# Kernel tuning notes

Measured on AMD Instinct MI355X. Metric: run time of the kernel, lower is better.

Reference implementation:

```python
import jax, jax.numpy as jnp
import numpy as np

NUM_USERS = 50000
NUM_ITEMS = 50000
N = NUM_USERS + NUM_ITEMS
EMBED_K = 64
N_LAYERS = 3
FEAT = 2048
N_EDGES = 2000000
BATCH = 8192
LEAKY_SLOPE = 0.2


def _l2norm(x):
    # torch F.normalize(p=2, dim=1): x / max(||x||, 1e-12)
    return x / jnp.maximum(jnp.linalg.norm(x, axis=1, keepdims=True), 1e-12)


def setup_inputs():
    key = jax.random.key(0)
    ks = jax.random.split(key, 12)
    s = 1.0 / np.sqrt(EMBED_K)
    return {
        "Gu": jax.random.normal(ks[0], (NUM_USERS, EMBED_K), jnp.float32) * 0.1,
        "Gi": jax.random.normal(ks[1], (NUM_ITEMS, EMBED_K), jnp.float32) * 0.1,
        "Tu": jax.random.normal(ks[2], (NUM_USERS, EMBED_K), jnp.float32) * 0.1,
        "F": jax.random.uniform(ks[3], (NUM_ITEMS, FEAT), jnp.float32),
        "proj_w": jax.random.normal(ks[4], (EMBED_K, FEAT), jnp.float32) / np.sqrt(FEAT),
        "proj_b": jnp.zeros((EMBED_K,), jnp.float32),
        "W1": jax.random.normal(ks[5], (N_LAYERS, EMBED_K, EMBED_K), jnp.float32) * s,
        "b1": jnp.zeros((N_LAYERS, EMBED_K), jnp.float32),
        "W2": jax.random.normal(ks[6], (N_LAYERS, EMBED_K, EMBED_K), jnp.float32) * s,
        "b2": jnp.zeros((N_LAYERS, EMBED_K), jnp.float32),
        "edge_weight": jax.random.uniform(ks[7], (N_EDGES,), jnp.float32) * 0.05,
        "edge_index": jax.random.randint(ks[8], (2, N_EDGES), 0, N, jnp.int32),
        "users": jax.random.randint(ks[9], (BATCH,), 0, NUM_USERS, jnp.int32),
        "items": jax.random.randint(ks[10], (BATCH,), 0, NUM_ITEMS, jnp.int32),
    }


def _propagate(Gu, Gi, W1, b1, W2, b2, edge_weight, edge_index):
    src, dst = edge_index[0], edge_index[1]
    x = jnp.concatenate([Gu, Gi], axis=0)  # [N, d]
    embs = [x]
    for l in range(N_LAYERS):
        # sparse adjacency aggregation: agg = A_hat @ x
        msg = x[src] * edge_weight[:, None]              # [E, d]
        agg = jax.ops.segment_sum(msg, dst, num_segments=N)  # [N, d]
        # NGCF layer: W1(x + agg) + W2(x * agg), leaky relu
        h = (x + agg) @ W1[l].T + b1[l] + (x * agg) @ W2[l].T + b2[l]
        h = jax.nn.leaky_relu(h, LEAKY_SLOPE)
        # dropout p=0 (identity), then per-node L2 normalize
        h = _l2norm(h)
        embs.append(h)
        x = h
    all_e = jnp.mean(jnp.stack(embs, axis=1), axis=1)  # mean over layers
    return all_e[:NUM_USERS], all_e[NUM_USERS:]


def reference(Gu, Gi, Tu, F, proj_w, proj_b, W1, b1, W2, b2, edge_weight, edge_index, users, items):
    gu, gi = _propagate(Gu, Gi, W1, b1, W2, b2, edge_weight, edge_index)
    gamma_u = gu[users]          # [B, d]
    gamma_i = gi[items]          # [B, d]
    theta_u = Tu[users]          # [B, d]
    proj_i = _l2norm(F[items] @ proj_w.T + proj_b)  # [B, d]
    xui = jnp.sum(gamma_u * gamma_i, axis=1) + jnp.sum(theta_u * proj_i, axis=1)
    return xui
```

## Files before the change

### kernel.cpp

```cpp
#include <hip/hip_runtime.h>

#define NUSERS 50000
#define NITEMS 50000
#define NN (NUSERS + NITEMS)
#define KDIM 64
#define NLAYERS 3
#define FEAT 2048
#define NEDGES 2000000
#define BATCH 8192
#define SLOPE 0.2f

#define BSLOT 64
#define CNT_PAD 100352
#define XBLK 6250
#define CBLK 98
#define TBLK 512
#define NNK (NN * KDIM)

typedef __attribute__((ext_vector_type(8))) short bf16x8;
typedef __attribute__((ext_vector_type(4))) float f32x4;

union U8 {
    bf16x8 v;
    uint4 u;
};

__device__ __forceinline__ unsigned short f2bf(float f) {
    unsigned int u = __float_as_uint(f);
    unsigned int r = (u + 0x7fffu + ((u >> 16) & 1u)) >> 16;
    return (unsigned short)r;
}
__device__ __forceinline__ unsigned int pack2(float a, float b) {
    return (unsigned int)f2bf(a) | ((unsigned int)f2bf(b) << 16);
}
__device__ __forceinline__ float b2f(unsigned short h) {
    return __uint_as_float((unsigned int)h << 16);
}

__global__ __launch_bounds__(256) void setup_kernel(const float* __restrict__ Gu,
                                                    const float* __restrict__ Gi,
                                                    const float* __restrict__ pw,
                                                    unsigned short* __restrict__ xh,
                                                    int* __restrict__ cnt,
                                                    unsigned short* __restrict__ pwh) {
    int bx = blockIdx.x;
    if (bx < XBLK) {
        int i = bx * 256 + threadIdx.x;
        const int totalU = NUSERS * KDIM / 4;
        float4 v = (i < totalU) ? ((const float4*)Gu)[i] : ((const float4*)Gi)[i - totalU];
        ushort4 h;
        h.x = f2bf(v.x); h.y = f2bf(v.y); h.z = f2bf(v.z); h.w = f2bf(v.w);
        ((ushort4*)xh)[i] = h;
    } else if (bx < XBLK + CBLK) {
        int i = (bx - XBLK) * 256 + threadIdx.x;
        ((int4*)cnt)[i] = make_int4(0, 0, 0, 0);
    } else {
        int tid = (bx - XBLK - CBLK) * 256 + threadIdx.x;
        pwh[tid] = f2bf(pw[tid]);
    }
}

__global__ __launch_bounds__(256) void fill_fixed_kernel(const int* __restrict__ ei,
                                                         const float* __restrict__ ew,
                                                         int* __restrict__ cnt,
                                                         int2* __restrict__ bucket) {
    int e = blockIdx.x * blockDim.x + threadIdx.x;
    if (e >= NEDGES) return;
    int src = ei[e];
    int dst = ei[NEDGES + e];
    int slot = atomicAdd(&cnt[dst], 1);
    if (slot < BSLOT)
        bucket[((long long)dst << 6) + slot] = make_int2(src, __float_as_int(ew[e]));
}

__global__ __launch_bounds__(256) void agg_kernel(const unsigned short* __restrict__ xh,
                                                  const int2* __restrict__ bucket,
                                                  const int* __restrict__ cnt,
                                                  unsigned short* __restrict__ aggh) {
    int t = threadIdx.x;
    int lane = t & 63, wid = t >> 6;
    int g = lane >> 3, l8 = lane & 7;
    int n = (blockIdx.x * 4 + wid) * 8 + g;
    if (n >= NN) return;
    int m = cnt[n];
    if (m > BSLOT) m = BSLOT;
    const int2* bk = bucket + ((long long)n << 6);
    const uint4* x4 = (const uint4*)xh;
    float a0[8], a1[8], a2[8], a3[8];
#pragma unroll
    for (int q = 0; q < 8; ++q) { a0[q] = 0.f; a1[q] = 0.f; a2[q] = 0.f; a3[q] = 0.f; }
    int j = 0;
    for (; j + 4 <= m; j += 4) {
        int2 p0 = bk[j], p1 = bk[j + 1], p2 = bk[j + 2], p3 = bk[j + 3];
        uint4 u0 = x4[((long long)p0.x << 3) + l8];
        uint4 u1 = x4[((long long)p1.x << 3) + l8];
        uint4 u2 = x4[((long long)p2.x << 3) + l8];
        uint4 u3 = x4[((long long)p3.x << 3) + l8];
        float w0 = __int_as_float(p0.y), w1 = __int_as_float(p1.y);
        float w2 = __int_as_float(p2.y), w3 = __int_as_float(p3.y);
        a0[0] += w0 * __uint_as_float(u0.x << 16); a0[1] += w0 * __uint_as_float(u0.x & 0xFFFF0000u);
        a0[2] += w0 * __uint_as_float(u0.y << 16); a0[3] += w0 * __uint_as_float(u0.y & 0xFFFF0000u);
        a0[4] += w0 * __uint_as_float(u0.z << 16); a0[5] += w0 * __uint_as_float(u0.z & 0xFFFF0000u);
        a0[6] += w0 * __uint_as_float(u0.w << 16); a0[7] += w0 * __uint_as_float(u0.w & 0xFFFF0000u);
        a1[0] += w1 * __uint_as_float(u1.x << 16); a1[1] += w1 * __uint_as_float(u1.x & 0xFFFF0000u);
        a1[2] += w1 * __uint_as_float(u1.y << 16); a1[3] += w1 * __uint_as_float(u1.y & 0xFFFF0000u);
        a1[4] += w1 * __uint_as_float(u1.z << 16); a1[5] += w1 * __uint_as_float(u1.z & 0xFFFF0000u);
        a1[6] += w1 * __uint_as_float(u1.w << 16); a1[7] += w1 * __uint_as_float(u1.w & 0xFFFF0000u);
        a2[0] += w2 * __uint_as_float(u2.x << 16); a2[1] += w2 * __uint_as_float(u2.x & 0xFFFF0000u);
        a2[2] += w2 * __uint_as_float(u2.y << 16); a2[3] += w2 * __uint_as_float(u2.y & 0xFFFF0000u);
        a2[4] += w2 * __uint_as_float(u2.z << 16); a2[5] += w2 * __uint_as_float(u2.z & 0xFFFF0000u);
        a2[6] += w2 * __uint_as_float(u2.w << 16); a2[7] += w2 * __uint_as_float(u2.w & 0xFFFF0000u);
        a3[0] += w3 * __uint_as_float(u3.x << 16); a3[1] += w3 * __uint_as_float(u3.x & 0xFFFF0000u);
        a3[2] += w3 * __uint_as_float(u3.y << 16); a3[3] += w3 * __uint_as_float(u3.y & 0xFFFF0000u);
        a3[4] += w3 * __uint_as_float(u3.z << 16); a3[5] += w3 * __uint_as_float(u3.z & 0xFFFF0000u);
        a3[6] += w3 * __uint_as_float(u3.w << 16); a3[7] += w3 * __uint_as_float(u3.w & 0xFFFF0000u);
    }
    for (; j < m; ++j) {
        int2 p0 = bk[j];
        uint4 u0 = x4[((long long)p0.x << 3) + l8];
        float w0 = __int_as_float(p0.y);
        a0[0] += w0 * __uint_as_float(u0.x << 16); a0[1] += w0 * __uint_as_float(u0.x & 0xFFFF0000u);
        a0[2] += w0 * __uint_as_float(u0.y << 16); a0[3] += w0 * __uint_as_float(u0.y & 0xFFFF0000u);
        a0[4] += w0 * __uint_as_float(u0.z << 16); a0[5] += w0 * __uint_as_float(u0.z & 0xFFFF0000u);
        a0[6] += w0 * __uint_as_float(u0.w << 16); a0[7] += w0 * __uint_as_float(u0.w & 0xFFFF0000u);
    }
#pragma unroll
    for (int q = 0; q < 8; ++q) a0[q] = (a0[q] + a1[q]) + (a2[q] + a3[q]);
    uint4 o;
    o.x = pack2(a0[0], a0[1]); o.y = pack2(a0[2], a0[3]);
    o.z = pack2(a0[4], a0[5]); o.w = pack2(a0[6], a0[7]);
    *(uint4*)(aggh + (long long)n * KDIM + l8 * 8) = o;
}

__global__ __launch_bounds__(256) void gemm_layer_kernel(const unsigned short* __restrict__ xh_in,
                                                         const unsigned short* __restrict__ aggh,
                                                         const float* __restrict__ W1,
                                                         const float* __restrict__ b1,
                                                         const float* __restrict__ W2,
                                                         const float* __restrict__ b2,
                                                         unsigned short* __restrict__ xhout,
                                                         int layer) {
    __shared__ unsigned short sS[64 * 72];
    __shared__ unsigned short sP[64 * 72];
    __shared__ unsigned short sW1[64 * 72];
    __shared__ unsigned short sW2[64 * 72];
    int t = threadIdx.x;
    const float* W1g = W1 + (long long)layer * KDIM * KDIM;
    const float* W2g = W2 + (long long)layer * KDIM * KDIM;
    for (int idx = t; idx < KDIM * KDIM; idx += 256) {
        int j = idx >> 6, k = idx & 63;
        sW1[j * 72 + k] = f2bf(W1g[idx]);
        sW2[j * 72 + k] = f2bf(W2g[idx]);
    }
    int n0 = blockIdx.x * 64;
    {
        int r = t >> 2, q = t & 3;
        int node = n0 + r;
        unsigned short* dS = &sS[r * 72 + q * 16];
        unsigned short* dP = &sP[r * 72 + q * 16];
        if (node < NN) {
            const unsigned short* xb = xh_in + (long long)node * KDIM + q * 16;
            const unsigned short* ab = aggh + (long long)node * KDIM + q * 16;
            uint4 hx = *(const uint4*)xb;
            uint4 hx2 = *(const uint4*)(xb + 8);
            uint4 ha = *(const uint4*)ab;
            uint4 ha2 = *(const uint4*)(ab + 8);
            uint4 swv, pwv, swv2, pwv2;
#define PROC(XW, AW, SW, PW)                                                        \
            {                                                                       \
                float xx0 = __uint_as_float((XW) << 16);                            \
                float xx1 = __uint_as_float((XW) & 0xFFFF0000u);                    \
                float aa0 = __uint_as_float((AW) << 16);                            \
                float aa1 = __uint_as_float((AW) & 0xFFFF0000u);                    \
                SW = pack2(xx0 + aa0, xx1 + aa1);                                   \
                PW = pack2(xx0 * aa0, xx1 * aa1);                                   \
            }
            PROC(hx.x, ha.x, swv.x, pwv.x)
            PROC(hx.y, ha.y, swv.y, pwv.y)
            PROC(hx.z, ha.z, swv.z, pwv.z)
            PROC(hx.w, ha.w, swv.w, pwv.w)
            PROC(hx2.x, ha2.x, swv2.x, pwv2.x)
            PROC(hx2.y, ha2.y, swv2.y, pwv2.y)
            PROC(hx2.z, ha2.z, swv2.z, pwv2.z)
            PROC(hx2.w, ha2.w, swv2.w, pwv2.w)
#undef PROC
            *(uint4*)dS = swv;
            *(uint4*)(dS + 8) = swv2;
            *(uint4*)dP = pwv;
            *(uint4*)(dP + 8) = pwv2;
        } else {
            uint4 z = make_uint4(0, 0, 0, 0);
            *(uint4*)dS = z; *(uint4*)(dS + 8) = z;
            *(uint4*)dP = z; *(uint4*)(dP + 8) = z;
        }
    }
    __syncthreads();

    int l = t & 63, w = t >> 6, m16 = l & 15, g4 = l >> 4;
    f32x4 acc[4];
#pragma unroll
    for (int c = 0; c < 4; ++c) {
        float bb = b1[layer * KDIM + c * 16 + m16] + b2[layer * KDIM + c * 16 + m16];
        acc[c] = (f32x4){bb, bb, bb, bb};
    }
    const int abase = (w * 16 + m16) * 72;
#pragma unroll
    for (int kh = 0; kh < 2; ++kh) {
        int ko = kh * 32 + g4 * 8;
        bf16x8 aS = *(const bf16x8*)&sS[abase + ko];
        bf16x8 aP = *(const bf16x8*)&sP[abase + ko];
#pragma unroll
        for (int c = 0; c < 4; ++c) {
            bf16x8 bw1 = *(const bf16x8*)&sW1[(c * 16 + m16) * 72 + ko];
            acc[c] = __builtin_amdgcn_mfma_f32_16x16x32_bf16(aS, bw1, acc[c], 0, 0, 0);
            bf16x8 bw2 = *(const bf16x8*)&sW2[(c * 16 + m16) * 72 + ko];
            acc[c] = __builtin_amdgcn_mfma_f32_16x16x32_bf16(aP, bw2, acc[c], 0, 0, 0);
        }
    }

    float sq[4] = {0.f, 0.f, 0.f, 0.f};
#pragma unroll
    for (int c = 0; c < 4; ++c) {
#pragma unroll
        for (int reg = 0; reg < 4; ++reg) {
            float h = acc[c][reg];
            h = h > 0.f ? h : SLOPE * h;
            acc[c][reg] = h;
            sq[reg] += h * h;
        }
    }
#pragma unroll
    for (int reg = 0; reg < 4; ++reg) {
#pragma unroll
        for (int off = 1; off < 16; off <<= 1) sq[reg] += __shfl_xor(sq[reg], off);
        sq[reg] = 1.0f / fmaxf(sqrtf(sq[reg]), 1e-12f);
    }
#pragma unroll
    for (int reg = 0; reg < 4; ++reg) {
        int node = n0 + w * 16 + g4 * 4 + reg;
        if (node < NN) {
#pragma unroll
            for (int c = 0; c < 4; ++c)
                xhout[(long long)node * KDIM + c * 16 + m16] = f2bf(acc[c][reg] * sq[reg]);
        }
    }
}

__global__ __launch_bounds__(512) void proj_kernel(const float* __restrict__ F,
                                                   const unsigned short* __restrict__ pwh,
                                                   const float* __restrict__ pb,
                                                   const int* __restrict__ items,
                                                   float* __restrict__ projB) {
    __shared__ float lds[8][64][16];
    int t = threadIdx.x;
    int l = t & 63, w = t >> 6, m16 = l & 15, g4 = l >> 4;
    int i0 = blockIdx.x * 16;
    int item = items[i0 + m16];
    const float* frow = F + (long long)item * FEAT + g4 * 8;
    f32x4 acc[4];
#pragma unroll
    for (int c = 0; c < 4; ++c) acc[c] = (f32x4){0.f, 0.f, 0.f, 0.f};
    float4 fa[8], fb[8];
#pragma unroll
    for (int u = 0; u < 8; ++u) {
        const float* p = frow + (w * 8 + u) * 32;
        fa[u] = *(const float4*)p;
        fb[u] = *(const float4*)(p + 4);
    }
#pragma unroll
    for (int u = 0; u < 8; ++u) {
        U8 af;
        af.u = make_uint4(pack2(fa[u].x, fa[u].y), pack2(fa[u].z, fa[u].w),
                          pack2(fb[u].x, fb[u].y), pack2(fb[u].z, fb[u].w));
#pragma unroll
        for (int c = 0; c < 4; ++c) {
            bf16x8 bw = *(const bf16x8*)(pwh + (long long)(c * 16 + m16) * FEAT +
                                         (w * 8 + u) * 32 + g4 * 8);
            acc[c] = __builtin_amdgcn_mfma_f32_16x16x32_bf16(af.v, bw, acc[c], 0, 0, 0);
        }
    }
#pragma unroll
    for (int c = 0; c < 4; ++c)
#pragma unroll
        for (int reg = 0; reg < 4; ++reg) lds[w][l][c * 4 + reg] = acc[c][reg];
    __syncthreads();
    for (int e = t; e < 1024; e += 512) {
        int ll = e >> 4, v = e & 15;
        float s = lds[0][ll][v];
#pragma unroll
        for (int ww = 1; ww < 8; ++ww) s += lds[ww][ll][v];
        lds[0][ll][v] = s;
    }
    __syncthreads();
    if (w == 0) {
        float av[4][4];
        float sq[4] = {0.f, 0.f, 0.f, 0.f};
#pragma unroll
        for (int c = 0; c < 4; ++c) {
            float bb = pb[c * 16 + m16];
#pragma unroll
            for (int reg = 0; reg < 4; ++reg) {
                float h = lds[0][l][c * 4 + reg] + bb;
                av[c][reg] = h;
                sq[reg] += h * h;
            }
        }
#pragma unroll
        for (int reg = 0; reg < 4; ++reg) {
#pragma unroll
            for (int off = 1; off < 16; off <<= 1) sq[reg] += __shfl_xor(sq[reg], off);
            sq[reg] = 1.0f / fmaxf(sqrtf(sq[reg]), 1e-12f);
        }
#pragma unroll
        for (int reg = 0; reg < 4; ++reg) {
            int b = i0 + g4 * 4 + reg;
#pragma unroll
            for (int c = 0; c < 4; ++c)
                projB[(long long)b * KDIM + c * 16 + m16] = av[c][reg] * sq[reg];
        }
    }
}

__global__ __launch_bounds__(256) void final_kernel(const unsigned short* __restrict__ xh0,
                                                    const unsigned short* __restrict__ xh1,
                                                    const unsigned short* __restrict__ xh2,
                                                    const unsigned short* __restrict__ xh3,
                                                    const float* __restrict__ Tu,
                                                    const float* __restrict__ projB,
                                                    const int* __restrict__ users,
                                                    const int* __restrict__ items,
                                                    float* __restrict__ out) {
    int lane = threadIdx.x & 63;
    int wid = threadIdx.x >> 6;
    int b = blockIdx.x * 4 + wid;
    if (b >= BATCH) return;
    int u = users[b];
    int it = NUSERS + items[b];
    long long uo = (long long)u * KDIM + lane;
    long long io = (long long)it * KDIM + lane;
    float gu = b2f(xh0[uo]) + b2f(xh1[uo]) + b2f(xh2[uo]) + b2f(xh3[uo]);
    float gi = b2f(xh0[io]) + b2f(xh1[io]) + b2f(xh2[io]) + b2f(xh3[io]);
    float tu = Tu[(long long)u * KDIM + lane];
    float pi = projB[(long long)b * KDIM + lane];
    float v = gu * gi * (1.0f / 16.0f) + tu * pi;
#pragma unroll
    for (int off = 32; off > 0; off >>= 1) v += __shfl_xor(v, off);
    if (lane == 0) out[b] = v;
}

extern "C" void kernel_launch(void* const* d_in, const int* in_sizes, int n_in,
                              void* d_out, int out_size, void* d_ws, size_t ws_size,
                              hipStream_t stream) {
    const float* Gu = (const float*)d_in[0];
    const float* Gi = (const float*)d_in[1];
    const float* Tu = (const float*)d_in[2];
    const float* F = (const float*)d_in[3];
    const float* pw = (const float*)d_in[4];
    const float* pb = (const float*)d_in[5];
    const float* W1 = (const float*)d_in[6];
    const float* b1 = (const float*)d_in[7];
    const float* W2 = (const float*)d_in[8];
    const float* b2 = (const float*)d_in[9];
    const float* ew = (const float*)d_in[10];
    const int* ei = (const int*)d_in[11];
    const int* users = (const int*)d_in[12];
    const int* items = (const int*)d_in[13];
    float* out = (float*)d_out;

    float* projB = (float*)d_ws;
    int2* bucket = (int2*)(projB + (size_t)BATCH * KDIM);
    int* cnt = (int*)(bucket + (size_t)NN * BSLOT);
    unsigned short* aggh = (unsigned short*)(cnt + CNT_PAD);
    unsigned short* pwh = aggh + (size_t)NNK;
    unsigned short* xh0 = pwh + (size_t)KDIM * FEAT;
    unsigned short* xh1 = xh0 + (size_t)NNK;
    unsigned short* xh2 = xh1 + (size_t)NNK;
    unsigned short* xh3 = xh2 + (size_t)NNK;

    setup_kernel<<<XBLK + CBLK + TBLK, 256, 0, stream>>>(Gu, Gi, pw, xh0, cnt, pwh);
    fill_fixed_kernel<<<(NEDGES + 255) / 256, 256, 0, stream>>>(ei, ew, cnt, bucket);

    unsigned short* xs[4] = {xh0, xh1, xh2, xh3};
    for (int ll = 0; ll < NLAYERS; ++ll) {
        agg_kernel<<<(NN + 31) / 32, 256, 0, stream>>>(xs[ll], bucket, cnt, aggh);
        gemm_layer_kernel<<<(NN + 63) / 64, 256, 0, stream>>>(xs[ll], aggh, W1, b1, W2, b2,
                                                              xs[ll + 1], ll);
    }

    proj_kernel<<<BATCH / 16, 512, 0, stream>>>(F, pwh, pb, items, projB);
    final_kernel<<<BATCH / 4, 256, 0, stream>>>(xh0, xh1, xh2, xh3, Tu, projB, users, items, out);
}
```

Baseline: 352.2 us.

## Split neighbor loop across lanes in aggregation with shuffle reduction

The aggregation kernel now gives each node a whole wavefront: eight lane groups stride over its edges and the partial sums are combined with xor shuffles. Before, each node had one 8-lane group walking its edges serially. With about 20 edges per node, this gives more memory-level parallelism per wave and less load imbalance, at the cost of shuffle-reduction work and twice as many blocks. The projection-weight conversion in setup is also vectorized to float4 with a quarter of the blocks.

New measurement: 377.3 us. 1.07x slower.

```diff
diff --git a/kernel.cpp b/kernel.cpp
--- a/kernel.cpp
+++ b/kernel.cpp
@@ -14,7 +14,7 @@
 #define CNT_PAD 100352
 #define XBLK 6250
 #define CBLK 98
-#define TBLK 512
+#define TBLK 128
 #define NNK (NN * KDIM)
 
 typedef __attribute__((ext_vector_type(8))) short bf16x8;
@@ -55,8 +55,11 @@
         int i = (bx - XBLK) * 256 + threadIdx.x;
         ((int4*)cnt)[i] = make_int4(0, 0, 0, 0);
     } else {
-        int tid = (bx - XBLK - CBLK) * 256 + threadIdx.x;
-        pwh[tid] = f2bf(pw[tid]);
+        int i = (bx - XBLK - CBLK) * 256 + threadIdx.x;
+        float4 v = ((const float4*)pw)[i];
+        ushort4 h;
+        h.x = f2bf(v.x); h.y = f2bf(v.y); h.z = f2bf(v.z); h.w = f2bf(v.w);
+        ((ushort4*)pwh)[i] = h;
     }
 }
 
@@ -79,57 +82,46 @@
                                                   unsigned short* __restrict__ aggh) {
     int t = threadIdx.x;
     int lane = t & 63, wid = t >> 6;
-    int g = lane >> 3, l8 = lane & 7;
-    int n = (blockIdx.x * 4 + wid) * 8 + g;
-    if (n >= NN) return;
-    int m = cnt[n];
-    if (m > BSLOT) m = BSLOT;
-    const int2* bk = bucket + ((long long)n << 6);
+    int e8 = lane >> 3;
+    int l8 = lane & 7;
+    int nbase = (blockIdx.x * 4 + wid) * 4;
     const uint4* x4 = (const uint4*)xh;
-    float a0[8], a1[8], a2[8], a3[8];
-#pragma unroll
-    for (int q = 0; q < 8; ++q) { a0[q] = 0.f; a1[q] = 0.f; a2[q] = 0.f; a3[q] = 0.f; }
-    int j = 0;
-    for (; j + 4 <= m; j += 4) {
-        int2 p0 = bk[j], p1 = bk[j + 1], p2 = bk[j + 2], p3 = bk[j + 3];
-        uint4 u0 = x4[((long long)p0.x << 3) + l8];
-        uint4 u1 = x4[((long long)p1.x << 3) + l8];
-        uint4 u2 = x4[((long long)p2.x << 3) + l8];
-        uint4 u3 = x4[((long long)p3.x << 3) + l8];
-        float w0 = __int_as_float(p0.y), w1 = __int_as_float(p1.y);
-        float w2 = __int_as_float(p2.y), w3 = __int_as_float(p3.y);
-        a0[0] += w0 * __uint_as_float(u0.x << 16); a0[1] += w0 * __uint_as_float(u0.x & 0xFFFF0000u);
-        a0[2] += w0 * __uint_as_float(u0.y << 16); a0[3] += w0 * __uint_as_float(u0.y & 0xFFFF0000u);
-        a0[4] += w0 * __uint_as_float(u0.z << 16); a0[5] += w0 * __uint_as_float(u0.z & 0xFFFF0000u);
-        a0[6] += w0 * __uint_as_float(u0.w << 16); a0[7] += w0 * __uint_as_float(u0.w & 0xFFFF0000u);
-        a1[0] += w1 * __uint_as_float(u1.x << 16); a1[1] += w1 * __uint_as_float(u1.x & 0xFFFF0000u);
-        a1[2] += w1 * __uint_as_float(u1.y << 16); a1[3] += w1 * __uint_as_float(u1.y & 0xFFFF0000u);
-        a1[4] += w1 * __uint_as_float(u1.z << 16); a1[5] += w1 * __uint_as_float(u1.z & 0xFFFF0000u);
-        a1[6] += w1 * __uint_as_float(u1.w << 16); a1[7] += w1 * __uint_as_float(u1.w & 0xFFFF0000u);
-        a2[0] += w2 * __uint_as_float(u2.x << 16); a2[1] += w2 * __uint_as_float(u2.x & 0xFFFF0000u);
-        a2[2] += w2 * __uint_as_float(u2.y << 16); a2[3] += w2 * __uint_as_float(u2.y & 0xFFFF0000u);
-        a2[4] += w2 * __uint_as_float(u2.z << 16); a2[5] += w2 * __uint_as_float(u2.z & 0xFFFF0000u);
-        a2[6] += w2 * __uint_as_float(u2.w << 16); a2[7] += w2 * __uint_as_float(u2.w & 0xFFFF0000u);
-        a3[0] += w3 * __uint_as_float(u3.x << 16); a3[1] += w3 * __uint_as_float(u3.x & 0xFFFF0000u);
-        a3[2] += w3 * __uint_as_float(u3.y << 16); a3[3] += w3 * __uint_as_float(u3.y & 0xFFFF0000u);
-        a3[4] += w3 * __uint_as_float(u3.z << 16); a3[5] += w3 * __uint_as_float(u3.z & 0xFFFF0000u);
-        a3[6] += w3 * __uint_as_float(u3.w << 16); a3[7] += w3 * __uint_as_float(u3.w & 0xFFFF0000u);
-    }
-    for (; j < m; ++j) {
-        int2 p0 = bk[j];
-        uint4 u0 = x4[((long long)p0.x << 3) + l8];
-        float w0 = __int_as_float(p0.y);
-        a0[0] += w0 * __uint_as_float(u0.x << 16); a0[1] += w0 * __uint_as_float(u0.x & 0xFFFF0000u);
-        a0[2] += w0 * __uint_as_float(u0.y << 16); a0[3] += w0 * __uint_as_float(u0.y & 0xFFFF0000u);
-        a0[4] += w0 * __uint_as_float(u0.z << 16); a0[5] += w0 * __uint_as_float(u0.z & 0xFFFF0000u);
-        a0[6] += w0 * __uint_as_float(u0.w << 16); a0[7] += w0 * __uint_as_float(u0.w & 0xFFFF0000u);
-    }
-#pragma unroll
-    for (int q = 0; q < 8; ++q) a0[q] = (a0[q] + a1[q]) + (a2[q] + a3[q]);
-    uint4 o;
-    o.x = pack2(a0[0], a0[1]); o.y = pack2(a0[2], a0[3]);
-    o.z = pack2(a0[4], a0[5]); o.w = pack2(a0[6], a0[7]);
-    *(uint4*)(aggh + (long long)n * KDIM + l8 * 8) = o;
+#pragma unroll
+    for (int ni = 0; ni < 4; ++ni) {
+        int n = nbase + ni;
+        if (n >= NN) break;
+        int m = cnt[n];
+        if (m > BSLOT) m = BSLOT;
+        const int2* bk = bucket + ((long long)n << 6);
+        float a[8];
+#pragma unroll
+        for (int q = 0; q < 8; ++q) a[q] = 0.f;
+        for (int j = e8; j < m; j += 8) {
+            int2 p = bk[j];
+            uint4 u = x4[((long long)p.x << 3) + l8];
+            float w = __int_as_float(p.y);
+            a[0] += w * __uint_as_float(u.x << 16);
+            a[1] += w * __uint_as_float(u.x & 0xFFFF0000u);
+            a[2] += w * __uint_as_float(u.y << 16);
+            a[3] += w * __uint_as_float(u.y & 0xFFFF0000u);
+            a[4] += w * __uint_as_float(u.z << 16);
+            a[5] += w * __uint_as_float(u.z & 0xFFFF0000u);
+            a[6] += w * __uint_as_float(u.w << 16);
+            a[7] += w * __uint_as_float(u.w & 0xFFFF0000u);
+        }
+#pragma unroll
+        for (int q = 0; q < 8; ++q) {
+            a[q] += __shfl_xor(a[q], 8);
+            a[q] += __shfl_xor(a[q], 16);
+            a[q] += __shfl_xor(a[q], 32);
+        }
+        if (e8 == 0) {
+            uint4 o;
+            o.x = pack2(a[0], a[1]); o.y = pack2(a[2], a[3]);
+            o.z = pack2(a[4], a[5]); o.w = pack2(a[6], a[7]);
+            *(uint4*)(aggh + (long long)n * KDIM + l8 * 8) = o;
+        }
+    }
 }
 
 __global__ __launch_bounds__(256) void gemm_layer_kernel(const unsigned short* __restrict__ xh_in,
@@ -382,7 +374,7 @@
 
     unsigned short* xs[4] = {xh0, xh1, xh2, xh3};
     for (int ll = 0; ll < NLAYERS; ++ll) {
-        agg_kernel<<<(NN + 31) / 32, 256, 0, stream>>>(xs[ll], bucket, cnt, aggh);
+        agg_kernel<<<(NN + 15) / 16, 256, 0, stream>>>(xs[ll], bucket, cnt, aggh);
         gemm_layer_kernel<<<(NN + 63) / 64, 256, 0, stream>>>(xs[ll], aggh, W1, b1, W2, b2,
                                                               xs[ll + 1], ll);
     }
```

## Fuse item projection GEMM with first-layer aggregation in one launch

Applied to the files above, without the earlier changes.

Merges the projection kernel and the layer-0 aggregation into a single grid, where the first blocks run the MFMA projection and the rest aggregate neighbor embeddings. The aim is to overlap the independent, memory-heavy projection gather with the aggregation and to drop one kernel launch. The pw-to-bf16 conversion in setup is also vectorized to float4, which cuts its block count. Aggregation blocks now run at 512 threads with 64 nodes each, which may change occupancy for that phase.

Result: faster. 338.4 us (-3.9%).

```diff
diff --git a/kernel.cpp b/kernel.cpp
--- a/kernel.cpp
+++ b/kernel.cpp
@@ -14,8 +14,10 @@
 #define CNT_PAD 100352
 #define XBLK 6250
 #define CBLK 98
-#define TBLK 512
+#define TBLK 128
 #define NNK (NN * KDIM)
+#define PROJ_BLOCKS (BATCH / 16)
+#define AGG_BLOCKS ((NN + 63) / 64)
 
 typedef __attribute__((ext_vector_type(8))) short bf16x8;
 typedef __attribute__((ext_vector_type(4))) float f32x4;
@@ -55,8 +57,11 @@
         int i = (bx - XBLK) * 256 + threadIdx.x;
         ((int4*)cnt)[i] = make_int4(0, 0, 0, 0);
     } else {
-        int tid = (bx - XBLK - CBLK) * 256 + threadIdx.x;
-        pwh[tid] = f2bf(pw[tid]);
+        int i = (bx - XBLK - CBLK) * 256 + threadIdx.x;
+        float4 v = ((const float4*)pw)[i];
+        ushort4 h;
+        h.x = f2bf(v.x); h.y = f2bf(v.y); h.z = f2bf(v.z); h.w = f2bf(v.w);
+        ((ushort4*)pwh)[i] = h;
     }
 }
 
@@ -73,15 +78,10 @@
         bucket[((long long)dst << 6) + slot] = make_int2(src, __float_as_int(ew[e]));
 }
 
-__global__ __launch_bounds__(256) void agg_kernel(const unsigned short* __restrict__ xh,
-                                                  const int2* __restrict__ bucket,
-                                                  const int* __restrict__ cnt,
-                                                  unsigned short* __restrict__ aggh) {
-    int t = threadIdx.x;
-    int lane = t & 63, wid = t >> 6;
-    int g = lane >> 3, l8 = lane & 7;
-    int n = (blockIdx.x * 4 + wid) * 8 + g;
-    if (n >= NN) return;
+__device__ __forceinline__ void agg_node(const unsigned short* __restrict__ xh,
+                                         const int2* __restrict__ bucket,
+                                         const int* __restrict__ cnt,
+                                         unsigned short* __restrict__ aggh, int n, int l8) {
     int m = cnt[n];
     if (m > BSLOT) m = BSLOT;
     const int2* bk = bucket + ((long long)n << 6);
@@ -130,6 +130,102 @@
     o.x = pack2(a0[0], a0[1]); o.y = pack2(a0[2], a0[3]);
     o.z = pack2(a0[4], a0[5]); o.w = pack2(a0[6], a0[7]);
     *(uint4*)(aggh + (long long)n * KDIM + l8 * 8) = o;
+}
+
+__global__ __launch_bounds__(256) void agg_kernel(const unsigned short* __restrict__ xh,
+                                                  const int2* __restrict__ bucket,
+                                                  const int* __restrict__ cnt,
+                                                  unsigned short* __restrict__ aggh) {
+    int t = threadIdx.x;
+    int lane = t & 63, wid = t >> 6;
+    int g = lane >> 3, l8 = lane & 7;
+    int n = (blockIdx.x * 4 + wid) * 8 + g;
+    if (n >= NN) return;
+    agg_node(xh, bucket, cnt, aggh, n, l8);
+}
+
+__global__ __launch_bounds__(512) void proj_agg0_kernel(const float* __restrict__ F,
+                                                        const unsigned short* __restrict__ pwh,
+                                                        const float* __restrict__ pb,
+                                                        const int* __restrict__ items,
+                                                        float* __restrict__ projB,
+                                                        const unsigned short* __restrict__ xh,
+                                                        const int2* __restrict__ bucket,
+                                                        const int* __restrict__ cnt,
+                                                        unsigned short* __restrict__ aggh) {
+    __shared__ float lds[8][64][16];
+    int t = threadIdx.x;
+    int l = t & 63, w = t >> 6, m16 = l & 15, g4 = l >> 4;
+    if (blockIdx.x >= PROJ_BLOCKS) {
+        int n = (blockIdx.x - PROJ_BLOCKS) * 64 + w * 8 + (l >> 3);
+        if (n < NN) agg_node(xh, bucket, cnt, aggh, n, l & 7);
+        return;
+    }
+    int i0 = blockIdx.x * 16;
+    int item = items[i0 + m16];
+    const float* frow = F + (long long)item * FEAT + g4 * 8;
+    f32x4 acc[4];
+#pragma unroll
+    for (int c = 0; c < 4; ++c) acc[c] = (f32x4){0.f, 0.f, 0.f, 0.f};
+    float4 fa[8], fb[8];
+#pragma unroll
+    for (int u = 0; u < 8; ++u) {
+        const float* p = frow + (w * 8 + u) * 32;
+        fa[u] = *(const float4*)p;
+        fb[u] = *(const float4*)(p + 4);
+    }
+#pragma unroll
+    for (int u = 0; u < 8; ++u) {
+        U8 af;
+        af.u = make_uint4(pack2(fa[u].x, fa[u].y), pack2(fa[u].z, fa[u].w),
+                          pack2(fb[u].x, fb[u].y), pack2(fb[u].z, fb[u].w));
+#pragma unroll
+        for (int c = 0; c < 4; ++c) {
+            bf16x8 bw = *(const bf16x8*)(pwh + (long long)(c * 16 + m16) * FEAT +
+                                         (w * 8 + u) * 32 + g4 * 8);
+            acc[c] = __builtin_amdgcn_mfma_f32_16x16x32_bf16(af.v, bw, acc[c], 0, 0, 0);
+        }
+    }
+#pragma unroll
+    for (int c = 0; c < 4; ++c)
+#pragma unroll
+        for (int reg = 0; reg < 4; ++reg) lds[w][l][c * 4 + reg] = acc[c][reg];
+    __syncthreads();
+    for (int e = t; e < 1024; e += 512) {
+        int ll = e >> 4, v = e & 15;
+        float s = lds[0][ll][v];
+#pragma unroll
+        for (int ww = 1; ww < 8; ++ww) s += lds[ww][ll][v];
+        lds[0][ll][v] = s;
+    }
+    __syncthreads();
+    if (w == 0) {
+        float av[4][4];
+        float sq[4] = {0.f, 0.f, 0.f, 0.f};
+#pragma unroll
+        for (int c = 0; c < 4; ++c) {
+            float bb = pb[c * 16 + m16];
+#pragma unroll
+            for (int reg = 0; reg < 4; ++reg) {
+                float h = lds[0][l][c * 4 + reg] + bb;
+                av[c][reg] = h;
+                sq[reg] += h * h;
+            }
+        }
+#pragma unroll
+        for (int reg = 0; reg < 4; ++reg) {
+#pragma unroll
+            for (int off = 1; off < 16; off <<= 1) sq[reg] += __shfl_xor(sq[reg], off);
+            sq[reg] = 1.0f / fmaxf(sqrtf(sq[reg]), 1e-12f);
+        }
+#pragma unroll
+        for (int reg = 0; reg < 4; ++reg) {
+            int b = i0 + g4 * 4 + reg;
+#pragma unroll
+            for (int c = 0; c < 4; ++c)
+                projB[(long long)b * KDIM + c * 16 + m16] = av[c][reg] * sq[reg];
+        }
+    }
 }
 
 __global__ __launch_bounds__(256) void gemm_layer_kernel(const unsigned short* __restrict__ xh_in,
@@ -246,81 +342,6 @@
     }
 }
 
-__global__ __launch_bounds__(512) void proj_kernel(const float* __restrict__ F,
-                                                   const unsigned short* __restrict__ pwh,
-                                                   const float* __restrict__ pb,
-                                                   const int* __restrict__ items,
-                                                   float* __restrict__ projB) {
-    __shared__ float lds[8][64][16];
-    int t = threadIdx.x;
-    int l = t & 63, w = t >> 6, m16 = l & 15, g4 = l >> 4;
-    int i0 = blockIdx.x * 16;
-    int item = items[i0 + m16];
-    const float* frow = F + (long long)item * FEAT + g4 * 8;
-    f32x4 acc[4];
-#pragma unroll
-    for (int c = 0; c < 4; ++c) acc[c] = (f32x4){0.f, 0.f, 0.f, 0.f};
-    float4 fa[8], fb[8];
-#pragma unroll
-    for (int u = 0; u < 8; ++u) {
-        const float* p = frow + (w * 8 + u) * 32;
-        fa[u] = *(const float4*)p;
-        fb[u] = *(const float4*)(p + 4);
-    }
-#pragma unroll
-    for (int u = 0; u < 8; ++u) {
-        U8 af;
-        af.u = make_uint4(pack2(fa[u].x, fa[u].y), pack2(fa[u].z, fa[u].w),
-                          pack2(fb[u].x, fb[u].y), pack2(fb[u].z, fb[u].w));
-#pragma unroll
-        for (int c = 0; c < 4; ++c) {
-            bf16x8 bw = *(const bf16x8*)(pwh + (long long)(c * 16 + m16) * FEAT +
-                                         (w * 8 + u) * 32 + g4 * 8);
-            acc[c] = __builtin_amdgcn_mfma_f32_16x16x32_bf16(af.v, bw, acc[c], 0, 0, 0);
-        }
-    }
-#pragma unroll
-    for (int c = 0; c < 4; ++c)
-#pragma unroll
-        for (int reg = 0; reg < 4; ++reg) lds[w][l][c * 4 + reg] = acc[c][reg];
-    __syncthreads();
-    for (int e = t; e < 1024; e += 512) {
-        int ll = e >> 4, v = e & 15;
-        float s = lds[0][ll][v];
-#pragma unroll
-        for (int ww = 1; ww < 8; ++ww) s += lds[ww][ll][v];
-        lds[0][ll][v] = s;
-    }
-    __syncthreads();
-    if (w == 0) {
-        float av[4][4];
-        float sq[4] = {0.f, 0.f, 0.f, 0.f};
-#pragma unroll
-        for (int c = 0; c < 4; ++c) {
-            float bb = pb[c * 16 + m16];
-#pragma unroll
-            for (int reg = 0; reg < 4; ++reg) {
-                float h = lds[0][l][c * 4 + reg] + bb;
-                av[c][reg] = h;
-                sq[reg] += h * h;
-            }
-        }
-#pragma unroll
-        for (int reg = 0; reg < 4; ++reg) {
-#pragma unroll
-            for (int off = 1; off < 16; off <<= 1) sq[reg] += __shfl_xor(sq[reg], off);
-            sq[reg] = 1.0f / fmaxf(sqrtf(sq[reg]), 1e-12f);
-        }
-#pragma unroll
-        for (int reg = 0; reg < 4; ++reg) {
-            int b = i0 + g4 * 4 + reg;
-#pragma unroll
-            for (int c = 0; c < 4; ++c)
-                projB[(long long)b * KDIM + c * 16 + m16] = av[c][reg] * sq[reg];
-        }
-    }
-}
-
 __global__ __launch_bounds__(256) void final_kernel(const unsigned short* __restrict__ xh0,
                                                     const unsigned short* __restrict__ xh1,
                                                     const unsigned short* __restrict__ xh2,
@@ -380,13 +401,16 @@
     setup_kernel<<<XBLK + CBLK + TBLK, 256, 0, stream>>>(Gu, Gi, pw, xh0, cnt, pwh);
     fill_fixed_kernel<<<(NEDGES + 255) / 256, 256, 0, stream>>>(ei, ew, cnt, bucket);
 
+    proj_agg0_kernel<<<PROJ_BLOCKS + AGG_BLOCKS, 512, 0, stream>>>(F, pwh, pb, items, projB,
+                                                                   xh0, bucket, cnt, aggh);
+    gemm_layer_kernel<<<(NN + 63) / 64, 256, 0, stream>>>(xh0, aggh, W1, b1, W2, b2, xh1, 0);
+
     unsigned short* xs[4] = {xh0, xh1, xh2, xh3};
-    for (int ll = 0; ll < NLAYERS; ++ll) {
+    for (int ll = 1; ll < NLAYERS; ++ll) {
         agg_kernel<<<(NN + 31) / 32, 256, 0, stream>>>(xs[ll], bucket, cnt, aggh);
         gemm_layer_kernel<<<(NN + 63) / 64, 256, 0, stream>>>(xs[ll], aggh, W1, b1, W2, b2,
                                                               xs[ll + 1], ll);
     }
 
-    proj_kernel<<<BATCH / 16, 512, 0, stream>>>(F, pwh, pb, items, projB);
     final_kernel<<<BATCH / 4, 256, 0, stream>>>(xh0, xh1, xh2, xh3, Tu, projB, users, items, out);
 }
```

## Pack edge buckets into 32-bit words and fuse projection with edge fill

Applied to the files above, without the earlier changes.

Each bucket entry now packs the 17-bit source index and a 15-bit truncated bf16 weight into one 32-bit word instead of an int2. This halves bucket write and read traffic in the fill and the three aggregation passes. The item-projection GEMM now shares a launch with the edge bucket fill, which saves one kernel launch and lets the compute-bound projection overlap the atomic-bound fill. The pw conversion is vectorised to float4. Edge weights lose precision (bf16 without its sign bit), which is safe only because the weights are non-negative.

Result: faster. 333.8 us, median of 2 (-5.2%).

```diff
diff --git a/kernel.cpp b/kernel.cpp
--- a/kernel.cpp
+++ b/kernel.cpp
@@ -14,8 +14,10 @@
 #define CNT_PAD 100352
 #define XBLK 6250
 #define CBLK 98
-#define TBLK 512
+#define TBLK 128
 #define NNK (NN * KDIM)
+#define PROJ_BLOCKS (BATCH / 16)
+#define FILL_BLOCKS ((NEDGES + 511) / 512)
 
 typedef __attribute__((ext_vector_type(8))) short bf16x8;
 typedef __attribute__((ext_vector_type(4))) float f32x4;
@@ -55,26 +57,107 @@
         int i = (bx - XBLK) * 256 + threadIdx.x;
         ((int4*)cnt)[i] = make_int4(0, 0, 0, 0);
     } else {
-        int tid = (bx - XBLK - CBLK) * 256 + threadIdx.x;
-        pwh[tid] = f2bf(pw[tid]);
-    }
-}
-
-__global__ __launch_bounds__(256) void fill_fixed_kernel(const int* __restrict__ ei,
-                                                         const float* __restrict__ ew,
-                                                         int* __restrict__ cnt,
-                                                         int2* __restrict__ bucket) {
-    int e = blockIdx.x * blockDim.x + threadIdx.x;
-    if (e >= NEDGES) return;
-    int src = ei[e];
-    int dst = ei[NEDGES + e];
-    int slot = atomicAdd(&cnt[dst], 1);
-    if (slot < BSLOT)
-        bucket[((long long)dst << 6) + slot] = make_int2(src, __float_as_int(ew[e]));
+        int i = (bx - XBLK - CBLK) * 256 + threadIdx.x;
+        float4 v = ((const float4*)pw)[i];
+        ushort4 h;
+        h.x = f2bf(v.x); h.y = f2bf(v.y); h.z = f2bf(v.z); h.w = f2bf(v.w);
+        ((ushort4*)pwh)[i] = h;
+    }
+}
+
+__global__ __launch_bounds__(512) void proj_fill_kernel(const float* __restrict__ F,
+                                                        const unsigned short* __restrict__ pwh,
+                                                        const float* __restrict__ pb,
+                                                        const int* __restrict__ items,
+                                                        float* __restrict__ projB,
+                                                        const int* __restrict__ ei,
+                                                        const float* __restrict__ ew,
+                                                        int* __restrict__ cnt,
+                                                        unsigned int* __restrict__ bucket) {
+    __shared__ float lds[8][64][16];
+    int t = threadIdx.x;
+    if (blockIdx.x >= PROJ_BLOCKS) {
+        int e = (blockIdx.x - PROJ_BLOCKS) * 512 + t;
+        if (e < NEDGES) {
+            int src = ei[e];
+            int dst = ei[NEDGES + e];
+            int slot = atomicAdd(&cnt[dst], 1);
+            if (slot < BSLOT)
+                bucket[((long long)dst << 6) + slot] =
+                    ((unsigned int)src << 15) | ((unsigned int)f2bf(ew[e]) & 0x7FFFu);
+        }
+        return;
+    }
+    int l = t & 63, w = t >> 6, m16 = l & 15, g4 = l >> 4;
+    int i0 = blockIdx.x * 16;
+    int item = items[i0 + m16];
+    const float* frow = F + (long long)item * FEAT + g4 * 8;
+    f32x4 acc[4];
+#pragma unroll
+    for (int c = 0; c < 4; ++c) acc[c] = (f32x4){0.f, 0.f, 0.f, 0.f};
+    float4 fa[8], fb[8];
+#pragma unroll
+    for (int u = 0; u < 8; ++u) {
+        const float* p = frow + (w * 8 + u) * 32;
+        fa[u] = *(const float4*)p;
+        fb[u] = *(const float4*)(p + 4);
+    }
+#pragma unroll
+    for (int u = 0; u < 8; ++u) {
+        U8 af;
+        af.u = make_uint4(pack2(fa[u].x, fa[u].y), pack2(fa[u].z, fa[u].w),
+                          pack2(fb[u].x, fb[u].y), pack2(fb[u].z, fb[u].w));
+#pragma unroll
+        for (int c = 0; c < 4; ++c) {
+            bf16x8 bw = *(const bf16x8*)(pwh + (long long)(c * 16 + m16) * FEAT +
+                                         (w * 8 + u) * 32 + g4 * 8);
+            acc[c] = __builtin_amdgcn_mfma_f32_16x16x32_bf16(af.v, bw, acc[c], 0, 0, 0);
+        }
+    }
+#pragma unroll
+    for (int c = 0; c < 4; ++c)
+#pragma unroll
+        for (int reg = 0; reg < 4; ++reg) lds[w][l][c * 4 + reg] = acc[c][reg];
+    __syncthreads();
+    for (int e = t; e < 1024; e += 512) {
+        int ll = e >> 4, v = e & 15;
+        float s = lds[0][ll][v];
+#pragma unroll
+        for (int ww = 1; ww < 8; ++ww) s += lds[ww][ll][v];
+        lds[0][ll][v] = s;
+    }
+    __syncthreads();
+    if (w == 0) {
+        float av[4][4];
+        float sq[4] = {0.f, 0.f, 0.f, 0.f};
+#pragma unroll
+        for (int c = 0; c < 4; ++c) {
+            float bb = pb[c * 16 + m16];
+#pragma unroll
+            for (int reg = 0; reg < 4; ++reg) {
+                float h = lds[0][l][c * 4 + reg] + bb;
+                av[c][reg] = h;
+                sq[reg] += h * h;
+            }
+        }
+#pragma unroll
+        for (int reg = 0; reg < 4; ++reg) {
+#pragma unroll
+            for (int off = 1; off < 16; off <<= 1) sq[reg] += __shfl_xor(sq[reg], off);
+            sq[reg] = 1.0f / fmaxf(sqrtf(sq[reg]), 1e-12f);
+        }
+#pragma unroll
+        for (int reg = 0; reg < 4; ++reg) {
+            int b = i0 + g4 * 4 + reg;
+#pragma unroll
+            for (int c = 0; c < 4; ++c)
+                projB[(long long)b * KDIM + c * 16 + m16] = av[c][reg] * sq[reg];
+        }
+    }
 }
 
 __global__ __launch_bounds__(256) void agg_kernel(const unsigned short* __restrict__ xh,
-                                                  const int2* __restrict__ bucket,
+                                                  const unsigned int* __restrict__ bucket,
                                                   const int* __restrict__ cnt,
                                                   unsigned short* __restrict__ aggh) {
     int t = threadIdx.x;
@@ -84,20 +167,22 @@
     if (n >= NN) return;
     int m = cnt[n];
     if (m > BSLOT) m = BSLOT;
-    const int2* bk = bucket + ((long long)n << 6);
+    const unsigned int* bk = bucket + ((long long)n << 6);
     const uint4* x4 = (const uint4*)xh;
     float a0[8], a1[8], a2[8], a3[8];
 #pragma unroll
     for (int q = 0; q < 8; ++q) { a0[q] = 0.f; a1[q] = 0.f; a2[q] = 0.f; a3[q] = 0.f; }
     int j = 0;
     for (; j + 4 <= m; j += 4) {
-        int2 p0 = bk[j], p1 = bk[j + 1], p2 = bk[j + 2], p3 = bk[j + 3];
-        uint4 u0 = x4[((long long)p0.x << 3) + l8];
-        uint4 u1 = x4[((long long)p1.x << 3) + l8];
-        uint4 u2 = x4[((long long)p2.x << 3) + l8];
-        uint4 u3 = x4[((long long)p3.x << 3) + l8];
-        float w0 = __int_as_float(p0.y), w1 = __int_as_float(p1.y);
-        float w2 = __int_as_float(p2.y), w3 = __int_as_float(p3.y);
+        unsigned int p0 = bk[j], p1 = bk[j + 1], p2 = bk[j + 2], p3 = bk[j + 3];
+        uint4 u0 = x4[((long long)(p0 >> 15) << 3) + l8];
+        uint4 u1 = x4[((long long)(p1 >> 15) << 3) + l8];
+        uint4 u2 = x4[((long long)(p2 >> 15) << 3) + l8];
+        uint4 u3 = x4[((long long)(p3 >> 15) << 3) + l8];
+        float w0 = __uint_as_float((p0 & 0x7FFFu) << 16);
+        float w1 = __uint_as_float((p1 & 0x7FFFu) << 16);
+        float w2 = __uint_as_float((p2 & 0x7FFFu) << 16);
+        float w3 = __uint_as_float((p3 & 0x7FFFu) << 16);
         a0[0] += w0 * __uint_as_float(u0.x << 16); a0[1] += w0 * __uint_as_float(u0.x & 0xFFFF0000u);
         a0[2] += w0 * __uint_as_float(u0.y << 16); a0[3] += w0 * __uint_as_float(u0.y & 0xFFFF0000u);
         a0[4] += w0 * __uint_as_float(u0.z << 16); a0[5] += w0 * __uint_as_float(u0.z & 0xFFFF0000u);
@@ -116,9 +201,9 @@
         a3[6] += w3 * __uint_as_float(u3.w << 16); a3[7] += w3 * __uint_as_float(u3.w & 0xFFFF0000u);
     }
     for (; j < m; ++j) {
-        int2 p0 = bk[j];
-        uint4 u0 = x4[((long long)p0.x << 3) + l8];
-        float w0 = __int_as_float(p0.y);
+        unsigned int p0 = bk[j];
+        uint4 u0 = x4[((long long)(p0 >> 15) << 3) + l8];
+        float w0 = __uint_as_float((p0 & 0x7FFFu) << 16);
         a0[0] += w0 * __uint_as_float(u0.x << 16); a0[1] += w0 * __uint_as_float(u0.x & 0xFFFF0000u);
         a0[2] += w0 * __uint_as_float(u0.y << 16); a0[3] += w0 * __uint_as_float(u0.y & 0xFFFF0000u);
         a0[4] += w0 * __uint_as_float(u0.z << 16); a0[5] += w0 * __uint_as_float(u0.z & 0xFFFF0000u);
@@ -246,81 +331,6 @@
     }
 }
 
-__global__ __launch_bounds__(512) void proj_kernel(const float* __restrict__ F,
-                                                   const unsigned short* __restrict__ pwh,
-                                                   const float* __restrict__ pb,
-                                                   const int* __restrict__ items,
-                                                   float* __restrict__ projB) {
-    __shared__ float lds[8][64][16];
-    int t = threadIdx.x;
-    int l = t & 63, w = t >> 6, m16 = l & 15, g4 = l >> 4;
-    int i0 = blockIdx.x * 16;
-    int item = items[i0 + m16];
-    const float* frow = F + (long long)item * FEAT + g4 * 8;
-    f32x4 acc[4];
-#pragma unroll
-    for (int c = 0; c < 4; ++c) acc[c] = (f32x4){0.f, 0.f, 0.f, 0.f};
-    float4 fa[8], fb[8];
-#pragma unroll
-    for (int u = 0; u < 8; ++u) {
-        const float* p = frow + (w * 8 + u) * 32;
-        fa[u] = *(const float4*)p;
-        fb[u] = *(const float4*)(p + 4);
-    }
-#pragma unroll
-    for (int u = 0; u < 8; ++u) {
-        U8 af;
-        af.u = make_uint4(pack2(fa[u].x, fa[u].y), pack2(fa[u].z, fa[u].w),
-                          pack2(fb[u].x, fb[u].y), pack2(fb[u].z, fb[u].w));
-#pragma unroll
-        for (int c = 0; c < 4; ++c) {
-            bf16x8 bw = *(const bf16x8*)(pwh + (long long)(c * 16 + m16) * FEAT +
-                                         (w * 8 + u) * 32 + g4 * 8);
-            acc[c] = __builtin_amdgcn_mfma_f32_16x16x32_bf16(af.v, bw, acc[c], 0, 0, 0);
-        }
-    }
-#pragma unroll
-    for (int c = 0; c < 4; ++c)
-#pragma unroll
-        for (int reg = 0; reg < 4; ++reg) lds[w][l][c * 4 + reg] = acc[c][reg];
-    __syncthreads();
-    for (int e = t; e < 1024; e += 512) {
-        int ll = e >> 4, v = e & 15;
-        float s = lds[0][ll][v];
-#pragma unroll
-        for (int ww = 1; ww < 8; ++ww) s += lds[ww][ll][v];
-        lds[0][ll][v] = s;
-    }
-    __syncthreads();
-    if (w == 0) {
-        float av[4][4];
-        float sq[4] = {0.f, 0.f, 0.f, 0.f};
-#pragma unroll
-        for (int c = 0; c < 4; ++c) {
-            float bb = pb[c * 16 + m16];
-#pragma unroll
-            for (int reg = 0; reg < 4; ++reg) {
-                float h = lds[0][l][c * 4 + reg] + bb;
-                av[c][reg] = h;
-                sq[reg] += h * h;
-            }
-        }
-#pragma unroll
-        for (int reg = 0; reg < 4; ++reg) {
-#pragma unroll
-            for (int off = 1; off < 16; off <<= 1) sq[reg] += __shfl_xor(sq[reg], off);
-            sq[reg] = 1.0f / fmaxf(sqrtf(sq[reg]), 1e-12f);
-        }
-#pragma unroll
-        for (int reg = 0; reg < 4; ++reg) {
-            int b = i0 + g4 * 4 + reg;
-#pragma unroll
-            for (int c = 0; c < 4; ++c)
-                projB[(long long)b * KDIM + c * 16 + m16] = av[c][reg] * sq[reg];
-        }
-    }
-}
-
 __global__ __launch_bounds__(256) void final_kernel(const unsigned short* __restrict__ xh0,
                                                     const unsigned short* __restrict__ xh1,
                                                     const unsigned short* __restrict__ xh2,
@@ -368,7 +378,7 @@
     float* out = (float*)d_out;
 
     float* projB = (float*)d_ws;
-    int2* bucket = (int2*)(projB + (size_t)BATCH * KDIM);
+    unsigned int* bucket = (unsigned int*)(projB + (size_t)BATCH * KDIM);
     int* cnt = (int*)(bucket + (size_t)NN * BSLOT);
     unsigned short* aggh = (unsigned short*)(cnt + CNT_PAD);
     unsigned short* pwh = aggh + (size_t)NNK;
@@ -378,7 +388,8 @@
     unsigned short* xh3 = xh2 + (size_t)NNK;
 
     setup_kernel<<<XBLK + CBLK + TBLK, 256, 0, stream>>>(Gu, Gi, pw, xh0, cnt, pwh);
-    fill_fixed_kernel<<<(NEDGES + 255) / 256, 256, 0, stream>>>(ei, ew, cnt, bucket);
+    proj_fill_kernel<<<PROJ_BLOCKS + FILL_BLOCKS, 512, 0, stream>>>(F, pwh, pb, items, projB,
+                                                                    ei, ew, cnt, bucket);
 
     unsigned short* xs[4] = {xh0, xh1, xh2, xh3};
     for (int ll = 0; ll < NLAYERS; ++ll) {
@@ -387,6 +398,5 @@
                                                               xs[ll + 1], ll);
     }
 
-    proj_kernel<<<BATCH / 16, 512, 0, stream>>>(F, pwh, pb, items, projB);
     final_kernel<<<BATCH / 4, 256, 0, stream>>>(xh0, xh1, xh2, xh3, Tu, projB, users, items, out);
 }
```
